# Performance work log

Hardware: AMD Instinct MI355X
Metric: run time of the kernel (lower is better)

Reference implementation:

```python
import jax, jax.numpy as jnp
import numpy as np

HIDDEN = 512
N_LAYERS = 2
SEQ = 512
BATCH = 64
H2 = HIDDEN * 2  # 1024
D_IN = H2 * (N_LAYERS + 1)  # 3072


def setup_inputs() -> dict:
    key = jax.random.key(0)
    ks = jax.random.split(key, 4)
    state = jax.random.normal(ks[0], (N_LAYERS, BATCH, H2), dtype=jnp.float32)
    encoder_output = jax.random.normal(ks[1], (SEQ, BATCH, H2), dtype=jnp.float32)
    # fc1: xavier_normal with tanh gain (5/3); fc2: kaiming_normal
    xavier_std = (5.0 / 3.0) * np.sqrt(2.0 / (D_IN + H2))
    W1 = jax.random.normal(ks[2], (H2, D_IN), dtype=jnp.float32) * xavier_std
    b1 = jnp.zeros((H2,), dtype=jnp.float32)
    W2 = jax.random.normal(ks[3], (1, H2), dtype=jnp.float32) * np.sqrt(2.0 / H2)
    b2 = jnp.zeros((1,), dtype=jnp.float32)
    return {"state": state, "encoder_output": encoder_output,
            "W1": W1, "b1": b1, "W2": W2, "b2": b2}


def reference(state, encoder_output, W1, b1, W2, b2):
    S, B, h2 = encoder_output.shape
    # (n_layers, B, H2) -> (B, n_layers*H2), broadcast over seq
    st = jnp.transpose(state, (1, 0, 2)).reshape(B, -1)
    st = jnp.broadcast_to(st[:, None, :], (B, S, st.shape[-1]))
    enc = jnp.transpose(encoder_output, (1, 0, 2))  # (B, S, H2)
    concat = jnp.concatenate([st, enc], axis=2)      # (B, S, 3*H2)
    energy = jnp.tanh(jnp.einsum('bsd,hd->bsh', concat, W1) + b1)
    energy = (jnp.einsum('bsh,oh->bso', energy, W2) + b2)  # (B, S, 1)
    energy = jnp.transpose(energy, (0, 2, 1))        # (B, 1, S)
    alpha = jax.nn.softmax(energy, axis=2)           # (B, 1, S)
    context = jnp.einsum('bqs,bsh->qbh', alpha, enc)  # (1, B, H2)
    return context, alpha
```

## Files before the change

### kernel.cpp

```cpp
#include <hip/hip_runtime.h>
#include <hip/hip_bf16.h>
#include <stdint.h>

#define H2      1024
#define SEQ     512
#define BATCH   64
#define M_TOTAL (SEQ * BATCH)

typedef __attribute__((ext_vector_type(8))) short short8;
typedef __attribute__((ext_vector_type(4))) float f32x4;

__device__ __forceinline__ unsigned pack2_bf16(float lo, float hi) {
    union { __hip_bfloat162 h; unsigned u; } v;
    v.h = __float22bfloat162_rn(make_float2(lo, hi));
    return v.u;
}

__device__ __forceinline__ float fast_tanh(float x) {
    float e = __expf(2.0f * x);
    return __fdividef(e - 1.0f, e + 1.0f);
}

__device__ __forceinline__ void gl_lds16(const unsigned short* g, unsigned short* l) {
    __builtin_amdgcn_global_load_lds(
        (const __attribute__((address_space(1))) unsigned int*)g,
        (__attribute__((address_space(3))) unsigned int*)l, 16, 0, 0);
}


__global__ __launch_bounds__(256) void k_setup(const float* __restrict__ W1,
                                               const float* __restrict__ b1,
                                               const float* __restrict__ state,
                                               const float* __restrict__ enc,
                                               unsigned short* __restrict__ W1e,
                                               unsigned short* __restrict__ encb,
                                               float* __restrict__ logits,
                                               float* __restrict__ sp) {
    __shared__ unsigned short T[16 * 1024];
    int blk = blockIdx.x, tid = threadIdx.x;
    int lane = tid & 63;
    if (blk < 512) {
        int gr = blk * 4 + (tid >> 6);
        int h  = ((gr >> 5) << 4) + (lane & 15);
        int k  = ((gr & 31) << 5) + ((lane >> 4) << 3);
        const float* src = W1 + (size_t)h * 3072 + 2048 + k;
        float4 v0 = *(const float4*)(src);
        float4 v1 = *(const float4*)(src + 4);
        uint4 o;
        o.x = pack2_bf16(v0.x, v0.y); o.y = pack2_bf16(v0.z, v0.w);
        o.z = pack2_bf16(v1.x, v1.y); o.w = pack2_bf16(v1.z, v1.w);
        *(uint4*)(W1e + (size_t)gr * 512 + lane * 8) = o;
    } else if (blk < 640) {
        logits[(blk - 512) * 256 + tid] = 0.f;
    } else if (blk < 704) {
        int mT   = blk - 640;
        int wave = tid >> 6;
        int c    = lane & 15;
        int kq   = (lane >> 4) << 3;
        int h    = mT * 16 + c;
        int b    = wave * 16 + c;
        const float* ap = W1 + (size_t)h * 3072 + kq;
        f32x4 acc = {0.f, 0.f, 0.f, 0.f};
        #pragma unroll 4
        for (int k0 = 0; k0 < 2048; k0 += 32) {
            int k = k0 + kq;
            float4 a0 = *(const float4*)(ap + k0);
            float4 a1 = *(const float4*)(ap + k0 + 4);
            int l = k >> 10, j = k & 1023;
            const float* bp = state + (((size_t)l * 64 + b) << 10) + j;
            float4 b0 = *(const float4*)bp;
            float4 b1v = *(const float4*)(bp + 4);
            union { short8 s; uint4 u; } fa, fb;
            fa.u.x = pack2_bf16(a0.x, a0.y); fa.u.y = pack2_bf16(a0.z, a0.w);
            fa.u.z = pack2_bf16(a1.x, a1.y); fa.u.w = pack2_bf16(a1.z, a1.w);
            fb.u.x = pack2_bf16(b0.x, b0.y); fb.u.y = pack2_bf16(b0.z, b0.w);
            fb.u.z = pack2_bf16(b1v.x, b1v.y); fb.u.w = pack2_bf16(b1v.z, b1v.w);
            acc = __builtin_amdgcn_mfma_f32_16x16x32_bf16(fa.s, fb.s, acc, 0, 0, 0);
        }
        int quad = lane >> 4;
        int bcol = wave * 16 + c;
        #pragma unroll
        for (int i = 0; i < 4; ++i) {
            int hh = mT * 16 + quad * 4 + i;
            sp[((size_t)bcol << 10) + hh] = acc[i] + b1[hh];
        }
    } else {
        int RB = blk - 704;
        const float*    src = enc  + (size_t)RB * 16384;
        unsigned short* dst = encb + (size_t)RB * 16384;

        float4 v[16];
        #pragma unroll
        for (int p = 0; p < 16; ++p)
            v[p] = *(const float4*)(src + p * 1024 + (tid << 2));
        #pragma unroll
        for (int p = 0; p < 16; ++p) {
            uint2 o;
            o.x = pack2_bf16(v[p].x, v[p].y);
            o.y = pack2_bf16(v[p].z, v[p].w);
            int byte = (p * 2048 + (tid << 3)) ^ ((p & 7) << 4);
            *(uint2*)((char*)T + byte) = o;
        }
        __syncthreads();

        #pragma unroll
        for (int q = 0; q < 8; ++q) {
            int cchunk = q * 256 + tid;
            int KC  = cchunk >> 6;
            int L   = cchunk & 63;
            int row = L & 15;
            int kb  = KC * 64 + ((L >> 4) << 4);
            int byte = (row * 2048 + kb) ^ ((row & 7) << 4);
            uint4 d = *(const uint4*)((const char*)T + byte);
            *(uint4*)(dst + (size_t)cchunk * 8) = d;
        }
    }
}

#define BM 128
#define BN 128
#define BK 32

__global__ __launch_bounds__(256, 2) void k_energy(const unsigned short* __restrict__ encb,
                                                   const unsigned short* __restrict__ W1e,
                                                   const float* __restrict__ sp,
                                                   const float* __restrict__ W2,
                                                   float* __restrict__ logits) {
    __shared__ unsigned short As[BM * BK];
    __shared__ unsigned short Bs[BN * BK];
    int bid = blockIdx.x;
    int c8  = bid & 7;
    int jj  = bid >> 3;
    int mT  = c8 * 32 + (jj >> 3);
    int nT  = jj & 7;
    int n0  = nT * BN;
    int m0  = mT * BM;
    int tid  = threadIdx.x;
    int lane = tid & 63, wave = tid >> 6;
    int wm   = (wave >> 1) << 6;
    int wn   = (wave & 1) << 6;

    int rg0 = wave * 2, rg1 = wave * 2 + 1;
    const unsigned short* gA0 = encb + ((size_t)(mT * 8 + rg0) * 32) * 512 + lane * 8;
    const unsigned short* gA1 = encb + ((size_t)(mT * 8 + rg1) * 32) * 512 + lane * 8;
    const unsigned short* gB0 = W1e  + ((size_t)(nT * 8 + rg0) * 32) * 512 + lane * 8;
    const unsigned short* gB1 = W1e  + ((size_t)(nT * 8 + rg1) * 32) * 512 + lane * 8;
    unsigned short* lA0 = As + rg0 * 512;
    unsigned short* lA1 = As + rg1 * 512;
    unsigned short* lB0 = Bs + rg0 * 512;
    unsigned short* lB1 = Bs + rg1 * 512;

    f32x4 acc[4][4];
    #pragma unroll
    for (int mi = 0; mi < 4; ++mi)
        #pragma unroll
        for (int ni = 0; ni < 4; ++ni)
            acc[mi][ni] = (f32x4){0.f, 0.f, 0.f, 0.f};

    int ablk = wm >> 4;
    int bblk = wn >> 4;
    const unsigned short* afb = As + ablk * 512 + lane * 8;
    const unsigned short* bfb = Bs + bblk * 512 + lane * 8;

    for (int k0 = 0; k0 < H2; k0 += BK) {
        int go = k0 * 16;
        __syncthreads();
        gl_lds16(gA0 + go, lA0);
        gl_lds16(gA1 + go, lA1);
        gl_lds16(gB0 + go, lB0);
        gl_lds16(gB1 + go, lB1);
        __syncthreads();
        short8 af[4], bf[4];
        #pragma unroll
        for (int i = 0; i < 4; ++i) {
            af[i] = *(const short8*)(afb + i * 512);
            bf[i] = *(const short8*)(bfb + i * 512);
        }
        #pragma unroll
        for (int mi = 0; mi < 4; ++mi)
            #pragma unroll
            for (int ni = 0; ni < 4; ++ni)
                acc[mi][ni] = __builtin_amdgcn_mfma_f32_16x16x32_bf16(af[mi], bf[ni], acc[mi][ni], 0, 0, 0);
    }

    int c    = lane & 15;
    int quad = lane >> 4;
    float w2v[4];
    int   hcol[4];
    #pragma unroll
    for (int ni = 0; ni < 4; ++ni) {
        hcol[ni] = n0 + wn + ni * 16 + c;
        w2v[ni]  = W2[hcol[ni]];
    }
    #pragma unroll
    for (int mi = 0; mi < 4; ++mi) {
        #pragma unroll
        for (int i = 0; i < 4; ++i) {
            int m = m0 + wm + mi * 16 + quad * 4 + i;
            int b = m & 63;
            const float* sprow = sp + ((size_t)b << 10);
            float t = 0.f;
            #pragma unroll
            for (int ni = 0; ni < 4; ++ni) {
                float e = acc[mi][ni][i] + sprow[hcol[ni]];
                t = fmaf(fast_tanh(e), w2v[ni], t);
            }
            t += __shfl_xor(t, 1);
            t += __shfl_xor(t, 2);
            t += __shfl_xor(t, 4);
            t += __shfl_xor(t, 8);
            if (c == 0) atomicAdd(logits + (size_t)b * 512 + (m >> 6), t);
        }
    }
}

__global__ __launch_bounds__(256) void k_softmax(const float* __restrict__ logits,
                                                 float* __restrict__ alpha) {
    int b = blockIdx.x;
    int tid = threadIdx.x;
    int lane = tid & 63, wave = tid >> 6;
    float v0 = logits[(size_t)b * 512 + tid];
    float v1 = logits[(size_t)b * 512 + 256 + tid];
    float mx = fmaxf(v0, v1);
    #pragma unroll
    for (int o = 32; o; o >>= 1) mx = fmaxf(mx, __shfl_xor(mx, o));
    __shared__ float redm[4];
    if (lane == 0) redm[wave] = mx;
    __syncthreads();
    mx = fmaxf(fmaxf(redm[0], redm[1]), fmaxf(redm[2], redm[3]));
    float e0 = __expf(v0 - mx), e1 = __expf(v1 - mx);
    float s = e0 + e1;
    #pragma unroll
    for (int o = 32; o; o >>= 1) s += __shfl_xor(s, o);
    __shared__ float reds[4];
    if (lane == 0) reds[wave] = s;
    __syncthreads();
    s = reds[0] + reds[1] + reds[2] + reds[3];
    float inv = 1.0f / s;
    alpha[(size_t)b * 512 + tid]       = e0 * inv;
    alpha[(size_t)b * 512 + 256 + tid] = e1 * inv;
}

#define NSC 32
__global__ __launch_bounds__(256) void k_context(const float* __restrict__ enc,
                                                 const float* __restrict__ alpha,
                                                 float* __restrict__ part) {
    int b  = blockIdx.x & 63;
    int sc = blockIdx.x >> 6;
    int h  = threadIdx.x << 2;
    float4 acc = make_float4(0.f, 0.f, 0.f, 0.f);
    int sbase = sc * 16;
    #pragma unroll
    for (int si = 0; si < 16; ++si) {
        int s = sbase + si;
        float a = alpha[(size_t)b * 512 + s];
        float4 e = *(const float4*)(enc + (((size_t)s * 64 + b) << 10) + h);
        acc.x = fmaf(a, e.x, acc.x);
        acc.y = fmaf(a, e.y, acc.y);
        acc.z = fmaf(a, e.z, acc.z);
        acc.w = fmaf(a, e.w, acc.w);
    }
    *(float4*)(part + (((size_t)sc * 64 + b) << 10) + h) = acc;
}

__global__ __launch_bounds__(256) void k_reduce(const float* __restrict__ part,
                                                float* __restrict__ ctx) {
    int b = blockIdx.x;
    int h = threadIdx.x << 2;
    float4 acc = make_float4(0.f, 0.f, 0.f, 0.f);
    #pragma unroll
    for (int sc = 0; sc < NSC; ++sc) {
        float4 p = *(const float4*)(part + (((size_t)sc * 64 + b) << 10) + h);
        acc.x += p.x; acc.y += p.y; acc.z += p.z; acc.w += p.w;
    }
    *(float4*)(ctx + ((size_t)b << 10) + h) = acc;
}

extern "C" void kernel_launch(void* const* d_in, const int* in_sizes, int n_in,
                              void* d_out, int out_size, void* d_ws, size_t ws_size,
                              hipStream_t stream) {
    const float* state = (const float*)d_in[0];
    const float* enc   = (const float*)d_in[1];
    const float* W1    = (const float*)d_in[2];
    const float* b1    = (const float*)d_in[3];
    const float* W2    = (const float*)d_in[4];

    float* ctx   = (float*)d_out;
    float* alpha = (float*)d_out + 65536;

    char* ws = (char*)d_ws;
    unsigned short* W1e    = (unsigned short*)(ws);
    float*          sp     = (float*)(ws + 2097152);
    float*          logits = (float*)(ws + 2097152 + 262144);
    unsigned short* encb   = (unsigned short*)(ws + 2097152 + 262144 + 131072);
    float*          part   = (float*)encb;

    k_setup<<<704 + 2048, 256, 0, stream>>>(W1, b1, state, enc, W1e, encb,
                                            logits, sp);
    k_energy<<<M_TOTAL / BM * (H2 / BN), 256, 0, stream>>>(encb, W1e, sp, W2, logits);
    k_softmax<<<64, 256, 0, stream>>>(logits, alpha);
    k_context<<<NSC * 64, 256, 0, stream>>>(enc, alpha, part);
    k_reduce<<<64, 256, 0, stream>>>(part, ctx);
}
```

Before: 345.0 us.

## Double GEMM K-tile to 64 and halve setup transpose LDS buffer

The energy GEMM now stages a K depth of 64 per iteration instead of 32. This halves the number of barrier pairs and loop iterations while issuing twice the MFMAs per sync. The setup kernel's encoder fp32-to-bf16 transpose now runs in two halves through a 16KB LDS buffer instead of 32KB, which may improve occupancy of that phase. The cost is more LDS per GEMM block and an extra barrier in the setup path.

```diff
diff --git a/kernel.cpp b/kernel.cpp
--- a/kernel.cpp
+++ b/kernel.cpp
@@ -36,7 +36,7 @@
                                                unsigned short* __restrict__ encb,
                                                float* __restrict__ logits,
                                                float* __restrict__ sp) {
-    __shared__ unsigned short T[16 * 1024];
+    __shared__ unsigned short T[16 * 512];
     int blk = blockIdx.x, tid = threadIdx.x;
     int lane = tid & 63;
     if (blk < 512) {
@@ -88,38 +88,41 @@
         int RB = blk - 704;
         const float*    src = enc  + (size_t)RB * 16384;
         unsigned short* dst = encb + (size_t)RB * 16384;
-
-        float4 v[16];
-        #pragma unroll
-        for (int p = 0; p < 16; ++p)
-            v[p] = *(const float4*)(src + p * 1024 + (tid << 2));
-        #pragma unroll
-        for (int p = 0; p < 16; ++p) {
-            uint2 o;
-            o.x = pack2_bf16(v[p].x, v[p].y);
-            o.y = pack2_bf16(v[p].z, v[p].w);
-            int byte = (p * 2048 + (tid << 3)) ^ ((p & 7) << 4);
-            *(uint2*)((char*)T + byte) = o;
-        }
-        __syncthreads();
-
-        #pragma unroll
-        for (int q = 0; q < 8; ++q) {
-            int cchunk = q * 256 + tid;
-            int KC  = cchunk >> 6;
-            int L   = cchunk & 63;
-            int row = L & 15;
-            int kb  = KC * 64 + ((L >> 4) << 4);
-            int byte = (row * 2048 + kb) ^ ((row & 7) << 4);
-            uint4 d = *(const uint4*)((const char*)T + byte);
-            *(uint4*)(dst + (size_t)cchunk * 8) = d;
+        int rhalf = tid >> 7;
+        int colq  = (tid & 127) << 2;
+        #pragma unroll
+        for (int h = 0; h < 2; ++h) {
+            if (h) __syncthreads();
+            #pragma unroll
+            for (int rp = 0; rp < 8; ++rp) {
+                int row = rp * 2 + rhalf;
+                float4 v = *(const float4*)(src + (size_t)row * 1024 + h * 512 + colq);
+                uint2 o;
+                o.x = pack2_bf16(v.x, v.y);
+                o.y = pack2_bf16(v.z, v.w);
+                int byte = (row * 1024 + colq * 2) ^ ((row & 7) << 4);
+                *(uint2*)((char*)T + byte) = o;
+            }
+            __syncthreads();
+            #pragma unroll
+            for (int q = 0; q < 4; ++q) {
+                int c   = q * 256 + tid;
+                int KCl = c >> 6;
+                int L   = c & 63;
+                int row = L & 15;
+                int kb  = KCl * 64 + ((L >> 4) << 4);
+                int byte = (row * 1024 + kb) ^ ((row & 7) << 4);
+                uint4 d = *(const uint4*)((const char*)T + byte);
+                *(uint4*)(dst + ((size_t)(h * 16 + KCl) * 512) + L * 8) = d;
+            }
         }
     }
 }
 
 #define BM 128
 #define BN 128
-#define BK 32
+#define BK 64
+#define KSTEPS (H2 / BK)
 
 __global__ __launch_bounds__(256, 2) void k_energy(const unsigned short* __restrict__ encb,
                                                    const unsigned short* __restrict__ W1e,
@@ -145,10 +148,14 @@
     const unsigned short* gA1 = encb + ((size_t)(mT * 8 + rg1) * 32) * 512 + lane * 8;
     const unsigned short* gB0 = W1e  + ((size_t)(nT * 8 + rg0) * 32) * 512 + lane * 8;
     const unsigned short* gB1 = W1e  + ((size_t)(nT * 8 + rg1) * 32) * 512 + lane * 8;
-    unsigned short* lA0 = As + rg0 * 512;
-    unsigned short* lA1 = As + rg1 * 512;
-    unsigned short* lB0 = Bs + rg0 * 512;
-    unsigned short* lB1 = Bs + rg1 * 512;
+    unsigned short* lA00 = As + (rg0 * 2 + 0) * 512;
+    unsigned short* lA01 = As + (rg0 * 2 + 1) * 512;
+    unsigned short* lA10 = As + (rg1 * 2 + 0) * 512;
+    unsigned short* lA11 = As + (rg1 * 2 + 1) * 512;
+    unsigned short* lB00 = Bs + (rg0 * 2 + 0) * 512;
+    unsigned short* lB01 = Bs + (rg0 * 2 + 1) * 512;
+    unsigned short* lB10 = Bs + (rg1 * 2 + 0) * 512;
+    unsigned short* lB11 = Bs + (rg1 * 2 + 1) * 512;
 
     f32x4 acc[4][4];
     #pragma unroll
@@ -159,28 +166,35 @@
 
     int ablk = wm >> 4;
     int bblk = wn >> 4;
-    const unsigned short* afb = As + ablk * 512 + lane * 8;
-    const unsigned short* bfb = Bs + bblk * 512 + lane * 8;
-
-    for (int k0 = 0; k0 < H2; k0 += BK) {
-        int go = k0 * 16;
+
+    for (int t = 0; t < KSTEPS; ++t) {
+        int go = t * 1024;
         __syncthreads();
-        gl_lds16(gA0 + go, lA0);
-        gl_lds16(gA1 + go, lA1);
-        gl_lds16(gB0 + go, lB0);
-        gl_lds16(gB1 + go, lB1);
+        gl_lds16(gA0 + go,       lA00);
+        gl_lds16(gA0 + go + 512, lA01);
+        gl_lds16(gA1 + go,       lA10);
+        gl_lds16(gA1 + go + 512, lA11);
+        gl_lds16(gB0 + go,       lB00);
+        gl_lds16(gB0 + go + 512, lB01);
+        gl_lds16(gB1 + go,       lB10);
+        gl_lds16(gB1 + go + 512, lB11);
         __syncthreads();
-        short8 af[4], bf[4];
+        short8 af[4][2], bf[4][2];
         #pragma unroll
         for (int i = 0; i < 4; ++i) {
-            af[i] = *(const short8*)(afb + i * 512);
-            bf[i] = *(const short8*)(bfb + i * 512);
+            #pragma unroll
+            for (int kh = 0; kh < 2; ++kh) {
+                af[i][kh] = *(const short8*)(As + ((ablk + i) * 2 + kh) * 512 + lane * 8);
+                bf[i][kh] = *(const short8*)(Bs + ((bblk + i) * 2 + kh) * 512 + lane * 8);
+            }
         }
         #pragma unroll
         for (int mi = 0; mi < 4; ++mi)
             #pragma unroll
-            for (int ni = 0; ni < 4; ++ni)
-                acc[mi][ni] = __builtin_amdgcn_mfma_f32_16x16x32_bf16(af[mi], bf[ni], acc[mi][ni], 0, 0, 0);
+            for (int ni = 0; ni < 4; ++ni) {
+                acc[mi][ni] = __builtin_amdgcn_mfma_f32_16x16x32_bf16(af[mi][0], bf[ni][0], acc[mi][ni], 0, 0, 0);
+                acc[mi][ni] = __builtin_amdgcn_mfma_f32_16x16x32_bf16(af[mi][1], bf[ni][1], acc[mi][ni], 0, 0, 0);
+            }
     }
 
     int c    = lane & 15;
```

Measured after the change: 379.4 us. 1.1x slower.

## Double-buffer LDS tiles in the energy GEMM main loop

Applied to the files above, without the earlier changes.

Doubles the shared-memory A/B tile buffers and prefetches the next K-slice with global_load_lds into the alternate buffer while the MFMAs consume the current one. The main loop now uses one barrier per iteration instead of two. The aim is to hide global-to-LDS load latency behind matrix-core work. In exchange, LDS use per block doubles, and the barrier at the end of each iteration may still wait on the in-flight prefetch, which limits how much overlap is gained.

```diff
diff --git a/kernel.cpp b/kernel.cpp
--- a/kernel.cpp
+++ b/kernel.cpp
@@ -120,14 +120,16 @@
 #define BM 128
 #define BN 128
 #define BK 32
+#define NT (H2 / BK)
+#define BUFSH (BM * BK)
 
 __global__ __launch_bounds__(256, 2) void k_energy(const unsigned short* __restrict__ encb,
                                                    const unsigned short* __restrict__ W1e,
                                                    const float* __restrict__ sp,
                                                    const float* __restrict__ W2,
                                                    float* __restrict__ logits) {
-    __shared__ unsigned short As[BM * BK];
-    __shared__ unsigned short Bs[BN * BK];
+    __shared__ unsigned short As[2 * BUFSH];
+    __shared__ unsigned short Bs[2 * BUFSH];
     int bid = blockIdx.x;
     int c8  = bid & 7;
     int jj  = bid >> 3;
@@ -145,10 +147,6 @@
     const unsigned short* gA1 = encb + ((size_t)(mT * 8 + rg1) * 32) * 512 + lane * 8;
     const unsigned short* gB0 = W1e  + ((size_t)(nT * 8 + rg0) * 32) * 512 + lane * 8;
     const unsigned short* gB1 = W1e  + ((size_t)(nT * 8 + rg1) * 32) * 512 + lane * 8;
-    unsigned short* lA0 = As + rg0 * 512;
-    unsigned short* lA1 = As + rg1 * 512;
-    unsigned short* lB0 = Bs + rg0 * 512;
-    unsigned short* lB1 = Bs + rg1 * 512;
 
     f32x4 acc[4][4];
     #pragma unroll
@@ -159,17 +157,28 @@
 
     int ablk = wm >> 4;
     int bblk = wn >> 4;
-    const unsigned short* afb = As + ablk * 512 + lane * 8;
-    const unsigned short* bfb = Bs + bblk * 512 + lane * 8;
-
-    for (int k0 = 0; k0 < H2; k0 += BK) {
-        int go = k0 * 16;
-        __syncthreads();
-        gl_lds16(gA0 + go, lA0);
-        gl_lds16(gA1 + go, lA1);
-        gl_lds16(gB0 + go, lB0);
-        gl_lds16(gB1 + go, lB1);
-        __syncthreads();
+
+    gl_lds16(gA0, As + rg0 * 512);
+    gl_lds16(gA1, As + rg1 * 512);
+    gl_lds16(gB0, Bs + rg0 * 512);
+    gl_lds16(gB1, Bs + rg1 * 512);
+    __syncthreads();
+
+    #pragma unroll 2
+    for (int t = 0; t < NT; ++t) {
+        const int cb = t & 1;
+        if (t + 1 < NT) {
+            int go = (t + 1) * 512;
+            unsigned short* An = As + (cb ^ 1) * BUFSH;
+            unsigned short* Bn = Bs + (cb ^ 1) * BUFSH;
+            gl_lds16(gA0 + go, An + rg0 * 512);
+            gl_lds16(gA1 + go, An + rg1 * 512);
+            gl_lds16(gB0 + go, Bn + rg0 * 512);
+            gl_lds16(gB1 + go, Bn + rg1 * 512);
+        }
+
+        const unsigned short* afb = As + cb * BUFSH + ablk * 512 + lane * 8;
+        const unsigned short* bfb = Bs + cb * BUFSH + bblk * 512 + lane * 8;
         short8 af[4], bf[4];
         #pragma unroll
         for (int i = 0; i < 4; ++i) {
@@ -181,6 +190,8 @@
             #pragma unroll
             for (int ni = 0; ni < 4; ++ni)
                 acc[mi][ni] = __builtin_amdgcn_mfma_f32_16x16x32_bf16(af[mi], bf[ni], acc[mi][ni], 0, 0, 0);
+
+        __syncthreads();
     }
 
     int c    = lane & 15;
```

Measured after the change: 348.7 us. Within noise of the previous version (+1.1%).
